# Optimization experiments

Measured on AMD Instinct MI355X. Metric: run time of the kernel, lower is better.

The kernel has to match this reference:

```python
import jax, jax.numpy as jnp
import numpy as np

D_IN = 1024
D_OUT = 1024
SEQ = 2048
BATCH = 4


def setup_inputs() -> dict:
    key = jax.random.key(0)
    k_x, k_q, k_k, k_v = jax.random.split(key, 4)
    scale = 1.0 / np.sqrt(D_IN)  # ~ torch Linear init scale
    x = jax.random.normal(k_x, (BATCH, SEQ, D_IN), dtype=jnp.float32)
    # torch nn.Linear weights have shape [d_out, d_in]; y = x @ W.T
    Wq = jax.random.uniform(k_q, (D_OUT, D_IN), jnp.float32, -scale, scale)
    Wk = jax.random.uniform(k_k, (D_OUT, D_IN), jnp.float32, -scale, scale)
    Wv = jax.random.uniform(k_v, (D_OUT, D_IN), jnp.float32, -scale, scale)
    return {"x": x, "Wq": Wq, "Wk": Wk, "Wv": Wv}


def reference(x, Wq, Wk, Wv):
    # projections (no bias, qkv_bias=False)
    q = jnp.einsum("bsd,ed->bse", x, Wq)  # [B,S,D_OUT]
    k = jnp.einsum("bsd,ed->bse", x, Wk)
    v = jnp.einsum("bsd,ed->bse", x, Wv)
    scores = jnp.einsum("bqe,bke->bqk", q, k)  # [B,S,S]
    seq = scores.shape[-1]
    causal = jnp.tril(jnp.ones((seq, seq), dtype=bool))  # keep lower-tri
    scores = jnp.where(causal[None], scores, -jnp.inf)
    # note: original scales AFTER masking: softmax(scores / sqrt(d_k))
    inv_sqrt_dk = 1.0 / np.sqrt(k.shape[-1]).astype(np.float32)
    weights = jax.nn.softmax(scores * inv_sqrt_dk, axis=-1)
    # dropout p=0.0 (eval-equivalent): identity
    return jnp.einsum("bqk,bke->bqe", weights, v)
```

## Files before the change

kernel.cpp:

```cpp
#include <hip/hip_runtime.h>
#include <hip/hip_bf16.h>

typedef __bf16 v8bf __attribute__((ext_vector_type(8)));
typedef float v4f __attribute__((ext_vector_type(4)));

#define GBL_AS(p) ((const __attribute__((address_space(1))) unsigned int*)(p))
#define LDS_AS(p) ((__attribute__((address_space(3))) unsigned int*)(p))

__global__ void cast_f32_bf16(const float* __restrict__ src,
                              __hip_bfloat16* __restrict__ dst, int n) {
  int i = (blockIdx.x * 256 + threadIdx.x) * 4;
  if (i >= n) return;
  float4 f = *(const float4*)(src + i);
  union { __hip_bfloat16 h[4]; uint2 u; } pk;
  pk.h[0] = __float2bfloat16(f.x);
  pk.h[1] = __float2bfloat16(f.y);
  pk.h[2] = __float2bfloat16(f.z);
  pk.h[3] = __float2bfloat16(f.w);
  *(uint2*)(dst + i) = pk.u;
}

__global__ void cast_w3(const float* __restrict__ a, const float* __restrict__ b,
                        const float* __restrict__ c, __hip_bfloat16* __restrict__ dst) {
  int seg = blockIdx.x >> 10;
  const float* src = seg == 0 ? a : (seg == 1 ? b : c);
  int i = ((blockIdx.x & 1023) * 256 + threadIdx.x) * 4;
  float4 f = *(const float4*)(src + i);
  union { __hip_bfloat16 h[4]; uint2 u; } pk;
  pk.h[0] = __float2bfloat16(f.x);
  pk.h[1] = __float2bfloat16(f.y);
  pk.h[2] = __float2bfloat16(f.z);
  pk.h[3] = __float2bfloat16(f.w);
  *(uint2*)(dst + seg * 1048576 + i) = pk.u;
}

__global__ void transpose_bf16(const __hip_bfloat16* __restrict__ src,
                               __hip_bfloat16* __restrict__ dst,
                               int rows, int cols) {
  __shared__ __hip_bfloat16 t[32][33];
  long boff = (long)blockIdx.z * rows * cols;
  src += boff; dst += boff;
  int c0 = blockIdx.x * 32, r0 = blockIdx.y * 32;
  int x = threadIdx.x;
#pragma unroll
  for (int i = 0; i < 4; ++i) {
    int y = threadIdx.y + i * 8;
    t[y][x] = src[(long)(r0 + y) * cols + (c0 + x)];
  }
  __syncthreads();
#pragma unroll
  for (int i = 0; i < 4; ++i) {
    int y = threadIdx.y + i * 8;
    dst[(long)(c0 + y) * rows + (r0 + x)] = t[x][y];
  }
}

template<int MODE>
__global__ __launch_bounds__(256, 2)
void gemm_nt(const __hip_bfloat16* __restrict__ A, long sAb, int lda,
             const __hip_bfloat16* __restrict__ B, long sBb, int ldb,
             void* __restrict__ Cv, long sCb, int ldc,
             int K, float scale, const float* __restrict__ inv_sums) {
  const int tid = threadIdx.x;
  const int l = tid & 63, w = tid >> 6;
  int z, nb;
  if (MODE == 0) { z = blockIdx.x >> 3; nb = (blockIdx.x & 7) << 7; }
  else           { z = blockIdx.z;      nb = blockIdx.x << 7; }
  const int mb = blockIdx.y * 128;
  if (MODE == 1 && nb > mb + 127) return;
  int kend = K;
  if (MODE == 2) kend = (K < mb + 128) ? K : (mb + 128);

  A += (long)z * sAb;
  B += (long)z * sBb;

  __shared__ alignas(16) __hip_bfloat16 As[128 * 32];
  __shared__ alignas(16) __hip_bfloat16 Bs[128 * 32];

  v4f acc[4][4] = {};
  const int wm = (w >> 1) * 64, wn = (w & 1) * 64;

  for (int k0 = 0; k0 < kend; k0 += 32) {
#pragma unroll
    for (int t = 0; t < 2; ++t) {
      const int cbase = t * 256 + w * 64;
      const int c = cbase + l;
      const int row = c >> 2, col = (c & 3) << 3;
      __builtin_amdgcn_global_load_lds(
          GBL_AS(A + (long)(mb + row) * lda + (k0 + col)),
          LDS_AS(As + cbase * 8), 16, 0, 0);
      __builtin_amdgcn_global_load_lds(
          GBL_AS(B + (long)(nb + row) * ldb + (k0 + col)),
          LDS_AS(Bs + cbase * 8), 16, 0, 0);
    }
    __syncthreads();

    v8bf af[4], bfr[4];
#pragma unroll
    for (int i = 0; i < 4; ++i) {
      af[i]  = *(const v8bf*)(As + (wm + i * 16 + (l & 15)) * 32 + ((l >> 4) << 3));
      bfr[i] = *(const v8bf*)(Bs + (wn + i * 16 + (l & 15)) * 32 + ((l >> 4) << 3));
    }
#pragma unroll
    for (int i = 0; i < 4; ++i)
#pragma unroll
      for (int j = 0; j < 4; ++j)
        acc[i][j] = __builtin_amdgcn_mfma_f32_16x16x32_bf16(af[i], bfr[j], acc[i][j], 0, 0, 0);
    __syncthreads();
  }

  const int col0 = nb + wn + (l & 15);
  const int row0 = mb + wm + ((l >> 4) << 2);
  if constexpr (MODE == 0) {
    __hip_bfloat16* C = (__hip_bfloat16*)Cv + (long)z * sCb;
#pragma unroll
    for (int i = 0; i < 4; ++i)
#pragma unroll
      for (int r = 0; r < 4; ++r) {
        long ro = (long)(row0 + i * 16 + r) * ldc;
#pragma unroll
        for (int j = 0; j < 4; ++j)
          C[ro + col0 + j * 16] = __float2bfloat16(acc[i][j][r] * scale);
      }
  } else if constexpr (MODE == 1) {
    __hip_bfloat16* C = (__hip_bfloat16*)Cv + (long)z * sCb;
#pragma unroll
    for (int i = 0; i < 4; ++i)
#pragma unroll
      for (int r = 0; r < 4; ++r) {
        const int m = row0 + i * 16 + r;
        long ro = (long)m * ldc;
#pragma unroll
        for (int j = 0; j < 4; ++j) {
          const int n = col0 + j * 16;
          float p = (n <= m) ? __expf(acc[i][j][r] * scale) : 0.0f;
          C[ro + n] = __float2bfloat16(p);
        }
      }
  } else {
    float* C = (float*)Cv + (long)z * sCb;
    const float* inv = inv_sums + z * 2048;
#pragma unroll
    for (int i = 0; i < 4; ++i)
#pragma unroll
      for (int r = 0; r < 4; ++r) {
        const int m = row0 + i * 16 + r;
        const float s = inv[m];
        long ro = (long)m * ldc;
#pragma unroll
        for (int j = 0; j < 4; ++j)
          C[ro + col0 + j * 16] = acc[i][j][r] * s;
      }
  }
}

__global__ __launch_bounds__(256)
void rowsum_inv(const __hip_bfloat16* __restrict__ P, float* __restrict__ inv) {
  const int w = threadIdx.x >> 6, l = threadIdx.x & 63;
  const int row = blockIdx.x * 4 + w;
  const int q = row & 2047;
  const int rend = ((q >> 7) + 1) << 7;
  const __hip_bfloat16* p = P + (long)row * 2048;
  float sum = 0.f;
  for (int c0 = l * 8; c0 < rend; c0 += 512) {
    union { v8bf v; unsigned short us[8]; } u;
    u.v = *(const v8bf*)(p + c0);
#pragma unroll
    for (int j = 0; j < 8; ++j)
      sum += __uint_as_float((unsigned)u.us[j] << 16);
  }
#pragma unroll
  for (int off = 32; off > 0; off >>= 1) sum += __shfl_down(sum, off);
  if (l == 0) inv[row] = 1.0f / sum;
}

extern "C" void kernel_launch(void* const* d_in, const int* in_sizes, int n_in,
                              void* d_out, int out_size, void* d_ws, size_t ws_size,
                              hipStream_t stream) {
  const float* x  = (const float*)d_in[0];
  const float* Wq = (const float*)d_in[1];
  const float* Wk = (const float*)d_in[2];
  const float* Wv = (const float*)d_in[3];
  float* out = (float*)d_out;
  char* ws = (char*)d_ws;

  __hip_bfloat16* qkv = (__hip_bfloat16*)ws;
  __hip_bfloat16* vT  = (__hip_bfloat16*)(ws + 50331648);
  __hip_bfloat16* xb  = (__hip_bfloat16*)(ws + 67108864);
  __hip_bfloat16* Wb  = (__hip_bfloat16*)(ws + 83886080);
  __hip_bfloat16* P   = (__hip_bfloat16*)(ws + 67108864);
  float* inv          = (float*)(ws + 100663296);

  cast_f32_bf16<<<8192, 256, 0, stream>>>(x, xb, 8388608);
  cast_w3<<<3072, 256, 0, stream>>>(Wq, Wk, Wv, Wb);

  gemm_nt<0><<<dim3(24, 64, 1), 256, 0, stream>>>(
      xb, 0L, 1024, Wb, 1048576L, 1024, qkv, 8388608L, 1024,
      1024, 1.0f, nullptr);

  transpose_bf16<<<dim3(32, 64, 4), dim3(32, 8), 0, stream>>>(
      qkv + 16777216, vT, 2048, 1024);

  gemm_nt<1><<<dim3(16, 16, 4), 256, 0, stream>>>(
      qkv, 2097152L, 1024, qkv + 8388608, 2097152L, 1024,
      P, 4194304L, 2048, 1024, 0.03125f, nullptr);

  rowsum_inv<<<2048, 256, 0, stream>>>(P, inv);

  gemm_nt<2><<<dim3(8, 16, 4), 256, 0, stream>>>(
      P, 4194304L, 2048, vT, 2097152L, 2048,
      out, 2097152L, 1024, 2048, 1.0f, inv);
}
```

Baseline: 263.6 us.

## Fuse softmax row sums into QK GEMM and compact causal block grids

The QK^T GEMM epilogue now reduces each row's exp values with shuffles and atomically adds them into a zeroed sums buffer. This removes the separate rowsum kernel and its re-read of P. The QK grid launches only the lower-triangular tiles, decoded with a sqrt-based index, instead of spawning and early-exiting upper tiles. The PV grid pairs short and long causal rows across batches to balance work. Launch bounds are raised to 4 blocks per CU, which risks register pressure, and float atomics add contention plus nondeterministic summation order.

```diff
diff --git a/kernel.cpp b/kernel.cpp
--- a/kernel.cpp
+++ b/kernel.cpp
@@ -56,20 +56,35 @@
 }
 
 template<int MODE>
-__global__ __launch_bounds__(256, 2)
+__global__ __launch_bounds__(256, 4)
 void gemm_nt(const __hip_bfloat16* __restrict__ A, long sAb, int lda,
              const __hip_bfloat16* __restrict__ B, long sBb, int ldb,
              void* __restrict__ Cv, long sCb, int ldc,
-             int K, float scale, const float* __restrict__ inv_sums) {
+             int K, float scale, float* __restrict__ sums) {
   const int tid = threadIdx.x;
   const int l = tid & 63, w = tid >> 6;
-  int z, nb;
-  if (MODE == 0) { z = blockIdx.x >> 3; nb = (blockIdx.x & 7) << 7; }
-  else           { z = blockIdx.z;      nb = blockIdx.x << 7; }
-  const int mb = blockIdx.y * 128;
-  if (MODE == 1 && nb > mb + 127) return;
-  int kend = K;
-  if (MODE == 2) kend = (K < mb + 128) ? K : (mb + 128);
+  int z, nb, mb, kend = K;
+  if (MODE == 0) {
+    z = blockIdx.x >> 3; nb = (blockIdx.x & 7) << 7; mb = blockIdx.y << 7;
+  } else if (MODE == 1) {
+    const int id = blockIdx.x;
+    z = id & 3;
+    const int t = id >> 2;
+    int m = (int)((__builtin_sqrtf(8.0f * t + 1.0f) - 1.0f) * 0.5f);
+    while ((m + 1) * (m + 2) / 2 <= t) ++m;
+    while (m * (m + 1) / 2 > t) --m;
+    mb = m << 7;
+    nb = (t - m * (m + 1) / 2) << 7;
+  } else {
+    const int id = blockIdx.x;
+    const int half = id >> 8, r8 = id & 255;
+    const int m = r8 >> 4, low = r8 & 15;
+    nb = (low >> 1) << 7;
+    z = (half << 1) | (low & 1);
+    const int mi = half ? (15 - m) : m;
+    mb = mi << 7;
+    kend = (mi + 1) << 7;
+  }
 
   A += (long)z * sAb;
   B += (long)z * sBb;
@@ -124,54 +139,42 @@
       }
   } else if constexpr (MODE == 1) {
     __hip_bfloat16* C = (__hip_bfloat16*)Cv + (long)z * sCb;
+    float* srow = sums + z * 2048;
 #pragma unroll
     for (int i = 0; i < 4; ++i)
 #pragma unroll
       for (int r = 0; r < 4; ++r) {
         const int m = row0 + i * 16 + r;
         long ro = (long)m * ldc;
+        float sp = 0.f;
 #pragma unroll
         for (int j = 0; j < 4; ++j) {
           const int n = col0 + j * 16;
           float p = (n <= m) ? __expf(acc[i][j][r] * scale) : 0.0f;
+          sp += p;
           C[ro + n] = __float2bfloat16(p);
         }
+        sp += __shfl_xor(sp, 1);
+        sp += __shfl_xor(sp, 2);
+        sp += __shfl_xor(sp, 4);
+        sp += __shfl_xor(sp, 8);
+        if ((l & 15) == 0) atomicAdd(&srow[m], sp);
       }
   } else {
     float* C = (float*)Cv + (long)z * sCb;
-    const float* inv = inv_sums + z * 2048;
+    const float* srow = sums + z * 2048;
 #pragma unroll
     for (int i = 0; i < 4; ++i)
 #pragma unroll
       for (int r = 0; r < 4; ++r) {
         const int m = row0 + i * 16 + r;
-        const float s = inv[m];
+        const float s = 1.0f / srow[m];
         long ro = (long)m * ldc;
 #pragma unroll
         for (int j = 0; j < 4; ++j)
           C[ro + col0 + j * 16] = acc[i][j][r] * s;
       }
   }
-}
-
-__global__ __launch_bounds__(256)
-void rowsum_inv(const __hip_bfloat16* __restrict__ P, float* __restrict__ inv) {
-  const int w = threadIdx.x >> 6, l = threadIdx.x & 63;
-  const int row = blockIdx.x * 4 + w;
-  const int q = row & 2047;
-  const int rend = ((q >> 7) + 1) << 7;
-  const __hip_bfloat16* p = P + (long)row * 2048;
-  float sum = 0.f;
-  for (int c0 = l * 8; c0 < rend; c0 += 512) {
-    union { v8bf v; unsigned short us[8]; } u;
-    u.v = *(const v8bf*)(p + c0);
-#pragma unroll
-    for (int j = 0; j < 8; ++j)
-      sum += __uint_as_float((unsigned)u.us[j] << 16);
-  }
-#pragma unroll
-  for (int off = 32; off > 0; off >>= 1) sum += __shfl_down(sum, off);
-  if (l == 0) inv[row] = 1.0f / sum;
 }
 
 extern "C" void kernel_launch(void* const* d_in, const int* in_sizes, int n_in,
@@ -189,7 +192,9 @@
   __hip_bfloat16* xb  = (__hip_bfloat16*)(ws + 67108864);
   __hip_bfloat16* Wb  = (__hip_bfloat16*)(ws + 83886080);
   __hip_bfloat16* P   = (__hip_bfloat16*)(ws + 67108864);
-  float* inv          = (float*)(ws + 100663296);
+  float* sums         = (float*)(ws + 100663296);
+
+  hipMemsetAsync(sums, 0, 8192 * sizeof(float), stream);
 
   cast_f32_bf16<<<8192, 256, 0, stream>>>(x, xb, 8388608);
   cast_w3<<<3072, 256, 0, stream>>>(Wq, Wk, Wv, Wb);
@@ -201,13 +206,11 @@
   transpose_bf16<<<dim3(32, 64, 4), dim3(32, 8), 0, stream>>>(
       qkv + 16777216, vT, 2048, 1024);
 
-  gemm_nt<1><<<dim3(16, 16, 4), 256, 0, stream>>>(
+  gemm_nt<1><<<dim3(544, 1, 1), 256, 0, stream>>>(
       qkv, 2097152L, 1024, qkv + 8388608, 2097152L, 1024,
-      P, 4194304L, 2048, 1024, 0.03125f, nullptr);
-
-  rowsum_inv<<<2048, 256, 0, stream>>>(P, inv);
-
-  gemm_nt<2><<<dim3(8, 16, 4), 256, 0, stream>>>(
+      P, 4194304L, 2048, 1024, 0.03125f, sums);
+
+  gemm_nt<2><<<dim3(512, 1, 1), 256, 0, stream>>>(
       P, 4194304L, 2048, vT, 2097152L, 2048,
-      out, 2097152L, 1024, 2048, 1.0f, inv);
-}
+      out, 2097152L, 1024, 2048, 1.0f, sums);
+}
```

New measurement: 245.2 us. 1.08x faster.
